# Optimization experiments

Measured on AMD Instinct MI355X. Metric: run time of the kernel, lower is better.

Reference implementation:

```python
import jax, jax.numpy as jnp
import numpy as np
import math

KV_STRIDE = 2
Q_STRIDE = 1
WAVE_LEN = 1000.0
POS_MAG = 1.0


def _pos_embed(h, w, h_kv, w_kv, q_stride, kv_stride, feat_dim):
    # Sinusoidal relative-position embeddings, matching get_position_embedding.
    h_idx = jnp.arange(h, dtype=jnp.float32) * q_stride
    w_idx = jnp.arange(w, dtype=jnp.float32) * q_stride
    h_kv_idx = jnp.arange(h_kv, dtype=jnp.float32) * kv_stride
    w_kv_idx = jnp.arange(w_kv, dtype=jnp.float32) * kv_stride
    h_diff = (h_idx[:, None] - h_kv_idx[None, :]) * POS_MAG  # (h, h_kv)
    w_diff = (w_idx[:, None] - w_kv_idx[None, :]) * POS_MAG  # (w, w_kv)
    feat_range = jnp.arange(feat_dim // 4, dtype=jnp.float32)
    dim_mat = WAVE_LEN ** (4.0 / feat_dim * feat_range)  # (feat_dim//4,)
    wd = w_diff[:, :, None] / dim_mat  # (w, w_kv, F)
    hd = h_diff[:, :, None] / dim_mat  # (h, h_kv, F)
    emb_x = jnp.concatenate([jnp.sin(wd), jnp.cos(wd)], axis=2)  # (w, w_kv, feat_dim//2)
    emb_y = jnp.concatenate([jnp.sin(hd), jnp.cos(hd)], axis=2)  # (h, h_kv, feat_dim//2)
    return emb_x, emb_y


def setup_inputs() -> dict:
    key = jax.random.key(0)
    ks = jax.random.split(key, 11)
    C = 288
    s = 1.0 / math.sqrt(C)
    return {
        'x_input': jax.random.normal(ks[0], (2, C, 64, 64), jnp.float32),
        'Wq': jax.random.normal(ks[1], (C, C), jnp.float32) * s,
        'Wk': jax.random.normal(ks[2], (C, C), jnp.float32) * s,
        'Wv': jax.random.normal(ks[3], (C, C), jnp.float32) * s,
        'Wx': jax.random.normal(ks[4], (C, C // 2), jnp.float32) * s,
        'Wy': jax.random.normal(ks[5], (C, C // 2), jnp.float32) * s,
        'Wproj': jax.random.normal(ks[6], (C, C), jnp.float32) * s,
        'bproj': jax.random.normal(ks[7], (C,), jnp.float32) * 0.02,
        'Wc': jax.random.normal(ks[8], (9, C), jnp.float32) * s,
        'bc': jax.random.normal(ks[9], (9,), jnp.float32) * 0.02,
        'gamma': jax.random.normal(ks[10], (1,), jnp.float32),
    }


def reference(x_input, Wq, Wk, Wv, Wx, Wy, Wproj, bproj, Wc, bc, gamma):
    M = Wc.shape[0]                       # num_mixtures
    n, C, h, w = x_input.shape
    d = Wq.shape[0] // M                  # qk_embed_dim (== v_dim)
    x_q = x_input                         # q_stride == 1
    x_kv = x_input[:, :, ::KV_STRIDE, ::KV_STRIDE]  # AvgPool2d(k=1, stride=2)
    h_kv, w_kv = x_kv.shape[2], x_kv.shape[3]

    # 1x1 convs as channel GEMMs
    q = jnp.einsum('nchw,oc->nohw', x_q, Wq).reshape(n, M, d, h * w)
    q = q.transpose(0, 1, 3, 2)                                    # (n,M,hw,d)
    k = jnp.einsum('nchw,oc->nohw', x_kv, Wk).reshape(n, M, d, h_kv * w_kv)

    emb_x, emb_y = _pos_embed(h, w, h_kv, w_kv, Q_STRIDE, KV_STRIDE, C)
    inv_sqrt2 = 1.0 / math.sqrt(2.0)
    pf_x = (emb_x @ Wx.T).reshape(w, w_kv, M, d).transpose(2, 0, 1, 3) * inv_sqrt2  # (M,w,w_kv,d)
    pf_y = (emb_y @ Wy.T).reshape(h, h_kv, M, d).transpose(2, 0, 1, 3) * inv_sqrt2  # (M,h,h_kv,d)

    energy = jnp.matmul(q, k).reshape(n, M, h, w, h_kv, w_kv)
    q5 = q.reshape(n, M, h, w, d)
    e_x = jnp.einsum('nmhwd,mwvd->nmhwv', q5, pf_x)  # (n,M,h,w,w_kv)
    e_y = jnp.einsum('nmhwd,mhud->nmhwu', q5, pf_y)  # (n,M,h,w,h_kv)
    energy = energy + e_x[:, :, :, :, None, :] + e_y[:, :, :, :, :, None]
    energy = energy.reshape(n, M, h * w, h_kv * w_kv)
    attn = jax.nn.softmax(energy, axis=3)

    # Learned per-mixture gating from mean query context
    context = q.transpose(0, 1, 3, 2).reshape(n, M * d, h * w).mean(axis=2)  # (n, M*d)
    mix_w = jax.nn.softmax(context @ Wc.T + bc, axis=1)                      # (n, M)
    attn = jnp.sum(attn * mix_w[:, :, None, None], axis=1)                   # (n,hw,hw_kv)

    v = jnp.einsum('nchw,oc->nohw', x_kv, Wv).reshape(n, M * d, h_kv * w_kv)
    v = v.transpose(0, 2, 1)                                                 # (n,hw_kv,M*d)
    out = jnp.matmul(attn, v).transpose(0, 2, 1).reshape(n, M * d, h, w)
    out = jnp.einsum('nchw,oc->nohw', out, Wproj) + bproj[None, :, None, None]
    return gamma[0] * out + x_input
```

## Files before the change

kernel.cpp:

```cpp
#include <hip/hip_runtime.h>
#include <math.h>

#define NB     2
#define CDIM   288
#define HW     4096
#define PKV    1024
#define MHEAD  9
#define DHEAD  32

typedef __attribute__((ext_vector_type(8))) short bf16x8;
typedef __attribute__((ext_vector_type(4))) float f32x4;

__device__ inline unsigned short f2bf(float x) {
    unsigned int u = __float_as_uint(x);
    u = (u + 0x7fffu + ((u >> 16) & 1u)) >> 16;
    return (unsigned short)u;
}


__global__ __launch_bounds__(256) void prep(const float* __restrict__ X,
        const float* __restrict__ Wq, const float* __restrict__ Wk,
        const float* __restrict__ Wv, const float* __restrict__ Wproj,
        const float* __restrict__ Wx, const float* __restrict__ Wy,
        unsigned short* __restrict__ XF, unsigned short* __restrict__ WFq,
        unsigned short* __restrict__ WFk, unsigned short* __restrict__ WFv,
        unsigned short* __restrict__ WFp, float* __restrict__ WTx,
        float* __restrict__ WTy, float* __restrict__ MX) {
    __shared__ float t32[32][33];
    __shared__ float t16[16][17];
    __shared__ float red[4];
    int b = blockIdx.x;
    int tid = threadIdx.x;
    if (b < 2304) {
        int bx = b % 128, by = (b / 128) % 9, n = b / 1152;
        int j0 = bx * 32, c0 = by * 32;
        int tx = tid & 31, ty = tid >> 5;
#pragma unroll
        for (int l = 0; l < 4; ++l) {
            int c = ty + l * 8;
            t32[c][tx] = X[((size_t)n * CDIM + c0 + c) * HW + j0 + tx];
        }
        __syncthreads();
        int s = tid >> 7;
        int u = tid & 127;
        int lane = u >> 1, e0 = (u & 1) * 4;
        int jl = s * 16 + (lane & 15);
        int cb = (lane >> 4) * 8 + e0;
        unsigned int w0 = f2bf(t32[cb + 0][jl]) | ((unsigned int)f2bf(t32[cb + 1][jl]) << 16);
        unsigned int w1 = f2bf(t32[cb + 2][jl]) | ((unsigned int)f2bf(t32[cb + 3][jl]) << 16);
        int jt = (j0 >> 4) + s, cc = c0 >> 5;
        unsigned short* O = XF + (size_t)n * HW * CDIM + ((size_t)jt * 9 + cc) * 512 + lane * 8 + e0;
        uint2 pk = { w0, w1 };
        *(uint2*)O = pk;
    } else if (b < 2628) {
        int u = b - 2304;
        int bx = u % 9, by = (u / 9) % 18, bz = u / 162;
        const float* W = bz ? Wy : Wx;
        float* WT      = bz ? WTy : WTx;
        int f0 = bx * 16, o0 = by * 16;
        int tx = tid & 15, ty = tid >> 4;
        t16[ty][tx] = W[(o0 + ty) * 144 + f0 + tx];
        __syncthreads();
        WT[(f0 + ty) * 288 + o0 + tx] = t16[tx][ty];
    } else if (b < 2790) {
        int t = b - 2628;
        int sub = tid >> 6, lane = tid & 63;
        int ot = t / 9, cc = t % 9;
        const float* W = (sub == 0) ? Wq : (sub == 1) ? Wk : (sub == 2) ? Wv : Wproj;
        unsigned short* O = ((sub == 0) ? WFq : (sub == 1) ? WFk : (sub == 2) ? WFv : WFp)
                            + (size_t)t * 512;
        int o  = ot * 16 + (lane & 15);
        int c0 = cc * 32 + (lane >> 4) * 8;
        const float* src = W + (size_t)o * CDIM + c0;
        float4 f0 = *(const float4*)src, f1 = *(const float4*)(src + 4);
        unsigned int v0 = f2bf(f0.x) | ((unsigned int)f2bf(f0.y) << 16);
        unsigned int v1 = f2bf(f0.z) | ((unsigned int)f2bf(f0.w) << 16);
        unsigned int v2 = f2bf(f1.x) | ((unsigned int)f2bf(f1.y) << 16);
        unsigned int v3 = f2bf(f1.z) | ((unsigned int)f2bf(f1.w) << 16);
        uint4 pk = { v0, v1, v2, v3 };
        *(uint4*)(O + lane * 8) = pk;
    } else {
        int bid = b - 2790;
        const float* xr = X + (size_t)bid * HW;
        float s = 0.f;
        for (int j = tid; j < HW; j += 256) s += xr[j];
        for (int off = 32; off > 0; off >>= 1) s += __shfl_xor(s, off, 64);
        if ((tid & 63) == 0) red[tid >> 6] = s;
        __syncthreads();
        if (tid == 0) MX[bid] = (red[0] + red[1] + red[2] + red[3]) * (1.f / 4096.f);
    }
}

__global__ __launch_bounds__(256) void qkv_F(const unsigned short* __restrict__ WFq,
        const unsigned short* __restrict__ WFk, const unsigned short* __restrict__ WFv,
        const unsigned short* __restrict__ XF, unsigned short* __restrict__ Qf,
        unsigned short* __restrict__ KF, unsigned short* __restrict__ VF) {
    __shared__ __attribute__((aligned(16))) unsigned short tr[4][32][40];
    int n  = blockIdx.z;
    int m  = blockIdx.y;
    int wv = threadIdx.x >> 6, lane = threadIdx.x & 63;
    int lq = lane & 15, quad = lane >> 4;
    if (blockIdx.x < 32) {
        int j0 = blockIdx.x * 128;
        int jw = j0 + wv * 32;
        const unsigned short* Wb = WFq + ((size_t)(m * 2) * 9) * 512 + lane * 8;
        const unsigned short* Xb = XF + (size_t)n * HW * CDIM + ((size_t)(jw >> 4) * 9) * 512 + lane * 8;
        f32x4 acc[2][2] = {};
#pragma unroll
        for (int cc = 0; cc < 9; ++cc) {
            bf16x8 a0 = *(const bf16x8*)(Wb + (size_t)cc * 512);
            bf16x8 a1 = *(const bf16x8*)(Wb + (size_t)(9 + cc) * 512);
            bf16x8 b0 = *(const bf16x8*)(Xb + (size_t)cc * 512);
            bf16x8 b1 = *(const bf16x8*)(Xb + (size_t)(9 + cc) * 512);
            acc[0][0] = __builtin_amdgcn_mfma_f32_16x16x32_bf16(a0, b0, acc[0][0], 0, 0, 0);
            acc[0][1] = __builtin_amdgcn_mfma_f32_16x16x32_bf16(a0, b1, acc[0][1], 0, 0, 0);
            acc[1][0] = __builtin_amdgcn_mfma_f32_16x16x32_bf16(a1, b0, acc[1][0], 0, 0, 0);
            acc[1][1] = __builtin_amdgcn_mfma_f32_16x16x32_bf16(a1, b1, acc[1][1], 0, 0, 0);
        }
#pragma unroll
        for (int oi = 0; oi < 2; ++oi)
#pragma unroll
            for (int ji = 0; ji < 2; ++ji)
#pragma unroll
                for (int r = 0; r < 4; ++r)
                    tr[wv][ji * 16 + lq][oi * 16 + quad * 4 + r] = f2bf(acc[oi][ji][r]);
        int jl = lane & 31, half = lane >> 5;
        bf16x8 v0 = *(const bf16x8*)&tr[wv][jl][half * 16];
        bf16x8 v1 = *(const bf16x8*)&tr[wv][jl][half * 16 + 8];
        unsigned short* Qm = Qf + ((size_t)(n * MHEAD + m) * HW + jw + jl) * 32 + half * 16;
        *(bf16x8*)Qm = v0;
        *(bf16x8*)(Qm + 8) = v1;
    } else {
        int p0 = (blockIdx.x - 32) * 128;
        int pw = p0 + wv * 32;
        const unsigned short* XFn = XF + (size_t)n * HW * CDIM;
        size_t bidx[2];
#pragma unroll
        for (int pi = 0; pi < 2; ++pi) {
            int p   = pw + pi * 16 + lq;
            int pos = ((p >> 5) << 7) + ((p & 31) << 1);
            bidx[pi] = ((size_t)(pos >> 4) * 9) * 512 + ((pos & 15) + 16 * quad) * 8;
        }
        const unsigned short* Wkb = WFk + ((size_t)(m * 2) * 9) * 512 + lane * 8;
        const unsigned short* Wvb = WFv + ((size_t)(m * 2) * 9) * 512 + lane * 8;
        f32x4 ak[2][2] = {}, av[2][2] = {};
#pragma unroll
        for (int cc = 0; cc < 9; ++cc) {
            bf16x8 a0k = *(const bf16x8*)(Wkb + (size_t)cc * 512);
            bf16x8 a1k = *(const bf16x8*)(Wkb + (size_t)(9 + cc) * 512);
            bf16x8 a0v = *(const bf16x8*)(Wvb + (size_t)cc * 512);
            bf16x8 a1v = *(const bf16x8*)(Wvb + (size_t)(9 + cc) * 512);
            bf16x8 b0  = *(const bf16x8*)(XFn + bidx[0] + (size_t)cc * 512);
            bf16x8 b1  = *(const bf16x8*)(XFn + bidx[1] + (size_t)cc * 512);
            ak[0][0] = __builtin_amdgcn_mfma_f32_16x16x32_bf16(a0k, b0, ak[0][0], 0, 0, 0);
            ak[0][1] = __builtin_amdgcn_mfma_f32_16x16x32_bf16(a0k, b1, ak[0][1], 0, 0, 0);
            ak[1][0] = __builtin_amdgcn_mfma_f32_16x16x32_bf16(a1k, b0, ak[1][0], 0, 0, 0);
            ak[1][1] = __builtin_amdgcn_mfma_f32_16x16x32_bf16(a1k, b1, ak[1][1], 0, 0, 0);
            av[0][0] = __builtin_amdgcn_mfma_f32_16x16x32_bf16(a0v, b0, av[0][0], 0, 0, 0);
            av[0][1] = __builtin_amdgcn_mfma_f32_16x16x32_bf16(a0v, b1, av[0][1], 0, 0, 0);
            av[1][0] = __builtin_amdgcn_mfma_f32_16x16x32_bf16(a1v, b0, av[1][0], 0, 0, 0);
            av[1][1] = __builtin_amdgcn_mfma_f32_16x16x32_bf16(a1v, b1, av[1][1], 0, 0, 0);
        }
#pragma unroll
        for (int oi = 0; oi < 2; ++oi)
#pragma unroll
            for (int pi = 0; pi < 2; ++pi)
#pragma unroll
                for (int r = 0; r < 4; ++r)
                    tr[wv][pi * 16 + lq][oi * 16 + quad * 4 + r] = f2bf(ak[oi][pi][r]);
        unsigned short* KFm = KF + (size_t)(n * MHEAD + m) * (PKV * 32);
#pragma unroll
        for (int pi = 0; pi < 2; ++pi) {
            bf16x8 v = *(const bf16x8*)&tr[wv][pi * 16 + lq][quad * 8];
            *(bf16x8*)(KFm + (size_t)((pw >> 4) + pi) * 512 + lane * 8) = v;
        }
#pragma unroll
        for (int oi = 0; oi < 2; ++oi)
#pragma unroll
            for (int pi = 0; pi < 2; ++pi)
#pragma unroll
                for (int r = 0; r < 4; ++r)
                    tr[wv][oi * 16 + quad * 4 + r][pi * 16 + lq] = f2bf(av[oi][pi][r]);
        unsigned short* VFn = VF + (size_t)n * CDIM * PKV;
#pragma unroll
        for (int oi = 0; oi < 2; ++oi) {
            bf16x8 v = *(const bf16x8*)&tr[wv][oi * 16 + lq][quad * 8];
            *(bf16x8*)(VFn + (size_t)((m * 2 + oi) * 32 + (pw >> 5)) * 512 + lane * 8) = v;
        }
    }
}

__global__ __launch_bounds__(320) void pff_kernel(const float* __restrict__ WTx,
        const float* __restrict__ WTy, float* __restrict__ FX, float* __restrict__ FY) {
    int blk  = blockIdx.x;
    int axis = blk / 126;
    int dif  = blk % 126;
    __shared__ float emb[144];
    int tid = threadIdx.x;
    float diff = (float)(dif - 62);
    if (tid < 72) {
        float dm = expf(6.9077552789821368f * ((float)tid * (1.f / 72.f)));
        float t  = diff / dm;
        emb[tid]      = sinf(t);
        emb[72 + tid] = cosf(t);
    }
    __syncthreads();
    if (tid < 288) {
        const float* WT = axis ? WTy : WTx;
        float s = 0.f;
#pragma unroll 8
        for (int f = 0; f < 144; ++f) s += emb[f] * WT[f * 288 + tid];
        int m = tid >> 5, d = tid & 31;
        float* F = axis ? FY : FX;
        F[((size_t)m * 126 + dif) * 32 + d] = s * 0.70710678118654752f;
    }
}

__global__ __launch_bounds__(256) void exey_kernel(const unsigned short* __restrict__ Qf,
        const float* __restrict__ FX, const float* __restrict__ FY,
        float* __restrict__ EX, float* __restrict__ EY) {
    int axis = blockIdx.x >> 6;
    int g    = blockIdx.x & 63;
    int m    = blockIdx.y;
    int n    = blockIdx.z;
    int tid  = threadIdx.x;
    size_t Qbase = (size_t)(n * MHEAD + m) * HW;

    __shared__ float fS[32][36];
    __shared__ unsigned int qSu[64][20];

    {
        const float* F = axis ? FY : FX;
        int v = tid >> 3, d0 = (tid & 7) * 4;
        *(float4*)&fS[v][d0] = *(const float4*)&F[((size_t)m * 126 + g + 62 - 2 * v) * 32 + d0];
    }
#pragma unroll
    for (int l = 0; l < 4; ++l) {
        int idx = tid + l * 256;
        int r = idx >> 4, c = idx & 15;
        int i = axis ? (g * 64 + r) : (r * 64 + g);
        qSu[r][c] = *(const unsigned int*)&Qf[(Qbase + i) * 32 + 2 * c];
    }
    __syncthreads();

    int r  = tid >> 2;
    int vg = tid & 3;
    float qv[32];
#pragma unroll
    for (int k = 0; k < 4; ++k) {
        uint4 qa = *(const uint4*)&qSu[r][k * 4];
        unsigned int uu[4] = { qa.x, qa.y, qa.z, qa.w };
#pragma unroll
        for (int e = 0; e < 4; ++e) {
            qv[k * 8 + 2 * e]     = __uint_as_float(uu[e] << 16);
            qv[k * 8 + 2 * e + 1] = __uint_as_float(uu[e] & 0xffff0000u);
        }
    }
    float acc8[8] = {};
#pragma unroll
    for (int k4 = 0; k4 < 8; ++k4) {
        float qx = qv[4 * k4], qy = qv[4 * k4 + 1], qz = qv[4 * k4 + 2], qw = qv[4 * k4 + 3];
#pragma unroll
        for (int t = 0; t < 8; ++t) {
            float4 f4 = *(const float4*)&fS[vg * 8 + t][k4 * 4];
            acc8[t] += qx * f4.x + qy * f4.y + qz * f4.z + qw * f4.w;
        }
    }
    int i = axis ? (g * 64 + r) : (r * 64 + g);
    float* out = axis ? EY : EX;
    size_t obase = (Qbase + i) * 32 + vg * 8;
    float4 s0 = { acc8[0], acc8[1], acc8[2], acc8[3] };
    float4 s1 = { acc8[4], acc8[5], acc8[6], acc8[7] };
    *(float4*)&out[obase]     = s0;
    *(float4*)&out[obase + 4] = s1;
}

__global__ void mixw2_kernel(const float* __restrict__ Wq, const float* __restrict__ MX,
                             const float* __restrict__ Wc, const float* __restrict__ bc,
                             float* __restrict__ MIXW) {
    __shared__ float ctx_s[NB * CDIM];
    __shared__ float lg[18];
    int tid = threadIdx.x;
    for (int p = tid; p < NB * CDIM; p += 256) {
        int n = p / CDIM, o = p % CDIM;
        const float* wr = Wq + (size_t)o * CDIM;
        const float* mx = MX + n * CDIM;
        float s = 0.f;
        for (int c = 0; c < CDIM; c += 4) {
            float4 w4 = *(const float4*)&wr[c];
            float4 m4 = *(const float4*)&mx[c];
            s += w4.x * m4.x + w4.y * m4.y + w4.z * m4.z + w4.w * m4.w;
        }
        ctx_s[p] = s;
    }
    __syncthreads();
    if (tid < 18) {
        int n = tid / 9, j = tid % 9;
        float s = bc[j];
        for (int o = 0; o < CDIM; ++o) s += ctx_s[n * CDIM + o] * Wc[j * CDIM + o];
        lg[tid] = s;
    }
    __syncthreads();
    if (tid < 2) {
        float mx = -1e30f;
        for (int j = 0; j < 9; ++j) mx = fmaxf(mx, lg[tid * 9 + j]);
        float e[9], sm = 0.f;
        for (int j = 0; j < 9; ++j) { e[j] = __expf(lg[tid * 9 + j] - mx); sm += e[j]; }
        for (int j = 0; j < 9; ++j) MIXW[tid * 9 + j] = e[j] / sm;
    }
}

__global__ __launch_bounds__(512, 4) void attn_fused(
        const unsigned short* __restrict__ Qf, const unsigned short* __restrict__ KF,
        const unsigned short* __restrict__ VF, const unsigned short* __restrict__ WFp,
        const float* __restrict__ EX, const float* __restrict__ EY,
        const float* __restrict__ MIXW, const float* __restrict__ bproj,
        const float* __restrict__ x, const float* __restrict__ gamma,
        float* __restrict__ OUT) {
    int n    = blockIdx.x >> 8;
    int i0   = (blockIdx.x & 255) * 16;
    int tid  = threadIdx.x;
    int wv   = tid >> 6;
    int lane = tid & 63;
    int lq   = lane & 15;
    int quad = lane >> 4;

    __shared__ float ext_s[16][33];
    __shared__ float eyt_s[16][33];
    __shared__ float ws_s[8][16];
    __shared__ float ltot_s[16];
    __shared__ __attribute__((aligned(16))) unsigned short tr[16][1032];
    __shared__ __attribute__((aligned(16))) unsigned short Mt[16][296];

    float mixed[8][4];
#pragma unroll
    for (int t = 0; t < 8; ++t)
#pragma unroll
        for (int j = 0; j < 4; ++j) mixed[t][j] = 0.f;

    int sq = tid >> 5, sv = tid & 31;

    for (int m = 0; m < MHEAD; ++m) {
        const unsigned short* Qm  = Qf + ((size_t)(n * MHEAD + m) * HW + i0) * 32;
        const unsigned short* KmF = KF + (size_t)(n * MHEAD + m) * (PKV * 32);
        size_t ebase = ((size_t)(n * MHEAD + m) * HW + i0 + sq) * 32 + sv;
        __syncthreads();
        ext_s[sq][sv] = EX[ebase];
        eyt_s[sq][sv] = EY[ebase];
        __syncthreads();

        bf16x8 afrag = *(const bf16x8*)(Qm + (size_t)lq * 32 + quad * 8);
        float exA[4], exB[4];
#pragma unroll
        for (int j = 0; j < 4; ++j) {
            exA[j] = ext_s[quad * 4 + j][lq];
            exB[j] = ext_s[quad * 4 + j][16 + lq];
        }

        bf16x8 bf[8];
#pragma unroll
        for (int t = 0; t < 8; ++t)
            bf[t] = *(const bf16x8*)(KmF + (size_t)(wv * 8 + t) * 512 + lane * 8);
        f32x4 acc[8];
#pragma unroll
        for (int t = 0; t < 8; ++t) acc[t] = (f32x4){0.f, 0.f, 0.f, 0.f};
#pragma unroll
        for (int t = 0; t < 8; ++t)
            acc[t] = __builtin_amdgcn_mfma_f32_16x16x32_bf16(afrag, bf[t], acc[t], 0, 0, 0);

        float rs[4] = {0.f, 0.f, 0.f, 0.f};
#pragma unroll
        for (int t = 0; t < 8; ++t) {
            int u = wv * 4 + (t >> 1);
            bool hi = t & 1;
#pragma unroll
            for (int j = 0; j < 4; ++j) {
                float e = __expf(acc[t][j] + (hi ? exB[j] : exA[j]) + eyt_s[quad * 4 + j][u]);
                rs[j] += e;
                acc[t][j] = e;
            }
        }
#pragma unroll
        for (int j = 0; j < 4; ++j) {
            rs[j] += __shfl_xor(rs[j], 1, 64);
            rs[j] += __shfl_xor(rs[j], 2, 64);
            rs[j] += __shfl_xor(rs[j], 4, 64);
            rs[j] += __shfl_xor(rs[j], 8, 64);
        }
        if (lq == 0) {
#pragma unroll
            for (int j = 0; j < 4; ++j) ws_s[wv][quad * 4 + j] = rs[j];
        }
        __syncthreads();
        if (tid < 16) {
            float s = 0.f;
#pragma unroll
            for (int w = 0; w < 8; ++w) s += ws_s[w][tid];
            ltot_s[tid] = s;
        }
        __syncthreads();

        float wm = MIXW[n * MHEAD + m];
        float fct[4];
#pragma unroll
        for (int j = 0; j < 4; ++j) fct[j] = wm / ltot_s[quad * 4 + j];
#pragma unroll
        for (int t = 0; t < 8; ++t)
#pragma unroll
            for (int j = 0; j < 4; ++j) mixed[t][j] += acc[t][j] * fct[j];
    }

#pragma unroll
    for (int t = 0; t < 8; ++t)
#pragma unroll
        for (int j = 0; j < 4; ++j)
            tr[quad * 4 + j][wv * 128 + t * 16 + lq] = f2bf(mixed[t][j]);
    __syncthreads();

    const unsigned short* VFn = VF + (size_t)n * CDIM * PKV;
    f32x4 accpv[3] = {};
#pragma unroll 4
    for (int pc = 0; pc < 32; ++pc) {
        bf16x8 pf = *(const bf16x8*)&tr[lq][pc * 32 + quad * 8];
#pragma unroll
        for (int idx = 0; idx < 3; ++idx) {
            int ot = wv + idx * 8;
            if (ot < 18) {
                bf16x8 vf = *(const bf16x8*)(VFn + (size_t)(ot * 32 + pc) * 512 + lane * 8);
                accpv[idx] = __builtin_amdgcn_mfma_f32_16x16x32_bf16(pf, vf, accpv[idx], 0, 0, 0);
            }
        }
    }
#pragma unroll
    for (int idx = 0; idx < 3; ++idx) {
        int ot = wv + idx * 8;
        if (ot < 18) {
#pragma unroll
            for (int r = 0; r < 4; ++r)
                Mt[quad * 4 + r][ot * 16 + lq] = f2bf(accpv[idx][r]);
        }
    }
    __syncthreads();

    float g = gamma[0];
#pragma unroll
    for (int idx = 0; idx < 3; ++idx) {
        int ot = wv + idx * 8;
        if (ot >= 18) continue;
        f32x4 acc = {};
#pragma unroll
        for (int cc = 0; cc < 9; ++cc) {
            bf16x8 af = *(const bf16x8*)(WFp + (size_t)(ot * 9 + cc) * 512 + lane * 8);
            bf16x8 bfm = *(const bf16x8*)&Mt[lq][cc * 32 + quad * 8];
            acc = __builtin_amdgcn_mfma_f32_16x16x32_bf16(af, bfm, acc, 0, 0, 0);
        }
#pragma unroll
        for (int r = 0; r < 4; ++r) {
            int o = ot * 16 + quad * 4 + r;
            size_t id = ((size_t)(n * CDIM) + o) * HW + i0 + lq;
            OUT[id] = g * (acc[r] + bproj[o]) + x[id];
        }
    }
}

extern "C" void kernel_launch(void* const* d_in, const int* in_sizes, int n_in,
                              void* d_out, int out_size, void* d_ws, size_t ws_size,
                              hipStream_t stream) {
    const float* x     = (const float*)d_in[0];
    const float* Wq    = (const float*)d_in[1];
    const float* Wk    = (const float*)d_in[2];
    const float* Wv    = (const float*)d_in[3];
    const float* Wx    = (const float*)d_in[4];
    const float* Wy    = (const float*)d_in[5];
    const float* Wproj = (const float*)d_in[6];
    const float* bproj = (const float*)d_in[7];
    const float* Wc    = (const float*)d_in[8];
    const float* bc    = (const float*)d_in[9];
    const float* gamma = (const float*)d_in[10];
    float* out = (float*)d_out;

    float* ws = (float*)d_ws;
    size_t off = 0;
    unsigned short* Qf  = (unsigned short*)(ws + off); off += (size_t)NB * MHEAD * HW * 32 / 2;
    unsigned short* KF  = (unsigned short*)(ws + off); off += (size_t)NB * MHEAD * PKV * 32 / 2;
    unsigned short* VF  = (unsigned short*)(ws + off); off += (size_t)NB * CDIM * PKV / 2;
    unsigned short* WFq = (unsigned short*)(ws + off); off += (size_t)CDIM * CDIM / 2;
    unsigned short* WFk = (unsigned short*)(ws + off); off += (size_t)CDIM * CDIM / 2;
    unsigned short* WFv = (unsigned short*)(ws + off); off += (size_t)CDIM * CDIM / 2;
    unsigned short* WFp = (unsigned short*)(ws + off); off += (size_t)CDIM * CDIM / 2;
    unsigned short* XF  = (unsigned short*)(ws + off); off += (size_t)NB * HW * CDIM / 2;
    float* WTx  = ws + off; off += 144 * 288;
    float* WTy  = ws + off; off += 144 * 288;
    float* FX   = ws + off; off += (size_t)MHEAD * 126 * 32;
    float* FY   = ws + off; off += (size_t)MHEAD * 126 * 32;
    float* EX   = ws + off; off += (size_t)NB * MHEAD * HW * 32;
    float* EY   = ws + off; off += (size_t)NB * MHEAD * HW * 32;
    float* MX   = ws + off; off += NB * CDIM;
    float* MIXW = ws + off; off += 32;

    prep<<<3366, 256, 0, stream>>>(x, Wq, Wk, Wv, Wproj, Wx, Wy,
                                   XF, WFq, WFk, WFv, WFp, WTx, WTy, MX);
    pff_kernel<<<252, 320, 0, stream>>>(WTx, WTy, FX, FY);
    mixw2_kernel<<<1, 256, 0, stream>>>(Wq, MX, Wc, bc, MIXW);
    qkv_F<<<dim3(40, MHEAD, NB), 256, 0, stream>>>(WFq, WFk, WFv, XF, Qf, KF, VF);
    exey_kernel<<<dim3(128, MHEAD, NB), 256, 0, stream>>>(Qf, FX, FY, EX, EY);
    attn_fused<<<NB * HW / 16, 512, 0, stream>>>(Qf, KF, VF, WFp, EX, EY, MIXW,
                                                 bproj, x, gamma, out);
}
```

Baseline: 205.1 us.

## Fuse prep-stage kernels and compute relative-position energies inside attention via MFMA

Merges the positional-feature projection, mixture-weight gating and QKV projection into one multi-role launch, cutting the launch count from six to three. The separate exey kernel and its large fp32 EX/EY buffers are removed. Instead each attention block multiplies its query fragment against bf16 position-feature tiles with MFMA and gathers the needed relative offsets from shared memory. This trades global-memory traffic and launches for extra MFMA work and shared-memory gathers inside the attention loop, and it also drops one barrier per head by summing row totals in every thread.

```diff
diff --git a/kernel.cpp b/kernel.cpp
--- a/kernel.cpp
+++ b/kernel.cpp
@@ -91,229 +91,180 @@
     }
 }
 
-__global__ __launch_bounds__(256) void qkv_F(const unsigned short* __restrict__ WFq,
-        const unsigned short* __restrict__ WFk, const unsigned short* __restrict__ WFv,
-        const unsigned short* __restrict__ XF, unsigned short* __restrict__ Qf,
-        unsigned short* __restrict__ KF, unsigned short* __restrict__ VF) {
-    __shared__ __attribute__((aligned(16))) unsigned short tr[4][32][40];
-    int n  = blockIdx.z;
-    int m  = blockIdx.y;
-    int wv = threadIdx.x >> 6, lane = threadIdx.x & 63;
-    int lq = lane & 15, quad = lane >> 4;
-    if (blockIdx.x < 32) {
-        int j0 = blockIdx.x * 128;
-        int jw = j0 + wv * 32;
-        const unsigned short* Wb = WFq + ((size_t)(m * 2) * 9) * 512 + lane * 8;
-        const unsigned short* Xb = XF + (size_t)n * HW * CDIM + ((size_t)(jw >> 4) * 9) * 512 + lane * 8;
-        f32x4 acc[2][2] = {};
-#pragma unroll
-        for (int cc = 0; cc < 9; ++cc) {
-            bf16x8 a0 = *(const bf16x8*)(Wb + (size_t)cc * 512);
-            bf16x8 a1 = *(const bf16x8*)(Wb + (size_t)(9 + cc) * 512);
-            bf16x8 b0 = *(const bf16x8*)(Xb + (size_t)cc * 512);
-            bf16x8 b1 = *(const bf16x8*)(Xb + (size_t)(9 + cc) * 512);
-            acc[0][0] = __builtin_amdgcn_mfma_f32_16x16x32_bf16(a0, b0, acc[0][0], 0, 0, 0);
-            acc[0][1] = __builtin_amdgcn_mfma_f32_16x16x32_bf16(a0, b1, acc[0][1], 0, 0, 0);
-            acc[1][0] = __builtin_amdgcn_mfma_f32_16x16x32_bf16(a1, b0, acc[1][0], 0, 0, 0);
-            acc[1][1] = __builtin_amdgcn_mfma_f32_16x16x32_bf16(a1, b1, acc[1][1], 0, 0, 0);
-        }
-#pragma unroll
-        for (int oi = 0; oi < 2; ++oi)
-#pragma unroll
-            for (int ji = 0; ji < 2; ++ji)
-#pragma unroll
-                for (int r = 0; r < 4; ++r)
-                    tr[wv][ji * 16 + lq][oi * 16 + quad * 4 + r] = f2bf(acc[oi][ji][r]);
-        int jl = lane & 31, half = lane >> 5;
-        bf16x8 v0 = *(const bf16x8*)&tr[wv][jl][half * 16];
-        bf16x8 v1 = *(const bf16x8*)&tr[wv][jl][half * 16 + 8];
-        unsigned short* Qm = Qf + ((size_t)(n * MHEAD + m) * HW + jw + jl) * 32 + half * 16;
-        *(bf16x8*)Qm = v0;
-        *(bf16x8*)(Qm + 8) = v1;
-    } else {
-        int p0 = (blockIdx.x - 32) * 128;
-        int pw = p0 + wv * 32;
-        const unsigned short* XFn = XF + (size_t)n * HW * CDIM;
-        size_t bidx[2];
-#pragma unroll
-        for (int pi = 0; pi < 2; ++pi) {
-            int p   = pw + pi * 16 + lq;
-            int pos = ((p >> 5) << 7) + ((p & 31) << 1);
-            bidx[pi] = ((size_t)(pos >> 4) * 9) * 512 + ((pos & 15) + 16 * quad) * 8;
-        }
-        const unsigned short* Wkb = WFk + ((size_t)(m * 2) * 9) * 512 + lane * 8;
-        const unsigned short* Wvb = WFv + ((size_t)(m * 2) * 9) * 512 + lane * 8;
-        f32x4 ak[2][2] = {}, av[2][2] = {};
-#pragma unroll
-        for (int cc = 0; cc < 9; ++cc) {
-            bf16x8 a0k = *(const bf16x8*)(Wkb + (size_t)cc * 512);
-            bf16x8 a1k = *(const bf16x8*)(Wkb + (size_t)(9 + cc) * 512);
-            bf16x8 a0v = *(const bf16x8*)(Wvb + (size_t)cc * 512);
-            bf16x8 a1v = *(const bf16x8*)(Wvb + (size_t)(9 + cc) * 512);
-            bf16x8 b0  = *(const bf16x8*)(XFn + bidx[0] + (size_t)cc * 512);
-            bf16x8 b1  = *(const bf16x8*)(XFn + bidx[1] + (size_t)cc * 512);
-            ak[0][0] = __builtin_amdgcn_mfma_f32_16x16x32_bf16(a0k, b0, ak[0][0], 0, 0, 0);
-            ak[0][1] = __builtin_amdgcn_mfma_f32_16x16x32_bf16(a0k, b1, ak[0][1], 0, 0, 0);
-            ak[1][0] = __builtin_amdgcn_mfma_f32_16x16x32_bf16(a1k, b0, ak[1][0], 0, 0, 0);
-            ak[1][1] = __builtin_amdgcn_mfma_f32_16x16x32_bf16(a1k, b1, ak[1][1], 0, 0, 0);
-            av[0][0] = __builtin_amdgcn_mfma_f32_16x16x32_bf16(a0v, b0, av[0][0], 0, 0, 0);
-            av[0][1] = __builtin_amdgcn_mfma_f32_16x16x32_bf16(a0v, b1, av[0][1], 0, 0, 0);
-            av[1][0] = __builtin_amdgcn_mfma_f32_16x16x32_bf16(a1v, b0, av[1][0], 0, 0, 0);
-            av[1][1] = __builtin_amdgcn_mfma_f32_16x16x32_bf16(a1v, b1, av[1][1], 0, 0, 0);
-        }
-#pragma unroll
-        for (int oi = 0; oi < 2; ++oi)
-#pragma unroll
-            for (int pi = 0; pi < 2; ++pi)
-#pragma unroll
-                for (int r = 0; r < 4; ++r)
-                    tr[wv][pi * 16 + lq][oi * 16 + quad * 4 + r] = f2bf(ak[oi][pi][r]);
-        unsigned short* KFm = KF + (size_t)(n * MHEAD + m) * (PKV * 32);
-#pragma unroll
-        for (int pi = 0; pi < 2; ++pi) {
-            bf16x8 v = *(const bf16x8*)&tr[wv][pi * 16 + lq][quad * 8];
-            *(bf16x8*)(KFm + (size_t)((pw >> 4) + pi) * 512 + lane * 8) = v;
-        }
-#pragma unroll
-        for (int oi = 0; oi < 2; ++oi)
-#pragma unroll
-            for (int pi = 0; pi < 2; ++pi)
-#pragma unroll
-                for (int r = 0; r < 4; ++r)
-                    tr[wv][oi * 16 + quad * 4 + r][pi * 16 + lq] = f2bf(av[oi][pi][r]);
-        unsigned short* VFn = VF + (size_t)n * CDIM * PKV;
-#pragma unroll
-        for (int oi = 0; oi < 2; ++oi) {
-            bf16x8 v = *(const bf16x8*)&tr[wv][oi * 16 + lq][quad * 8];
-            *(bf16x8*)(VFn + (size_t)((m * 2 + oi) * 32 + (pw >> 5)) * 512 + lane * 8) = v;
-        }
-    }
-}
-
-__global__ __launch_bounds__(320) void pff_kernel(const float* __restrict__ WTx,
-        const float* __restrict__ WTy, float* __restrict__ FX, float* __restrict__ FY) {
-    int blk  = blockIdx.x;
-    int axis = blk / 126;
-    int dif  = blk % 126;
+__global__ __launch_bounds__(256) void mid(
+        const float* __restrict__ WTx, const float* __restrict__ WTy,
+        unsigned short* __restrict__ FXb, unsigned short* __restrict__ FYb,
+        const float* __restrict__ Wq, const float* __restrict__ MX,
+        const float* __restrict__ Wc, const float* __restrict__ bc,
+        float* __restrict__ MIXW,
+        const unsigned short* __restrict__ WFq, const unsigned short* __restrict__ WFk,
+        const unsigned short* __restrict__ WFv, const unsigned short* __restrict__ XF,
+        unsigned short* __restrict__ Qf, unsigned short* __restrict__ KF,
+        unsigned short* __restrict__ VF) {
     __shared__ float emb[144];
-    int tid = threadIdx.x;
-    float diff = (float)(dif - 62);
-    if (tid < 72) {
-        float dm = expf(6.9077552789821368f * ((float)tid * (1.f / 72.f)));
-        float t  = diff / dm;
-        emb[tid]      = sinf(t);
-        emb[72 + tid] = cosf(t);
-    }
-    __syncthreads();
-    if (tid < 288) {
-        const float* WT = axis ? WTy : WTx;
-        float s = 0.f;
-#pragma unroll 8
-        for (int f = 0; f < 144; ++f) s += emb[f] * WT[f * 288 + tid];
-        int m = tid >> 5, d = tid & 31;
-        float* F = axis ? FY : FX;
-        F[((size_t)m * 126 + dif) * 32 + d] = s * 0.70710678118654752f;
-    }
-}
-
-__global__ __launch_bounds__(256) void exey_kernel(const unsigned short* __restrict__ Qf,
-        const float* __restrict__ FX, const float* __restrict__ FY,
-        float* __restrict__ EX, float* __restrict__ EY) {
-    int axis = blockIdx.x >> 6;
-    int g    = blockIdx.x & 63;
-    int m    = blockIdx.y;
-    int n    = blockIdx.z;
-    int tid  = threadIdx.x;
-    size_t Qbase = (size_t)(n * MHEAD + m) * HW;
-
-    __shared__ float fS[32][36];
-    __shared__ unsigned int qSu[64][20];
-
-    {
-        const float* F = axis ? FY : FX;
-        int v = tid >> 3, d0 = (tid & 7) * 4;
-        *(float4*)&fS[v][d0] = *(const float4*)&F[((size_t)m * 126 + g + 62 - 2 * v) * 32 + d0];
-    }
-#pragma unroll
-    for (int l = 0; l < 4; ++l) {
-        int idx = tid + l * 256;
-        int r = idx >> 4, c = idx & 15;
-        int i = axis ? (g * 64 + r) : (r * 64 + g);
-        qSu[r][c] = *(const unsigned int*)&Qf[(Qbase + i) * 32 + 2 * c];
-    }
-    __syncthreads();
-
-    int r  = tid >> 2;
-    int vg = tid & 3;
-    float qv[32];
-#pragma unroll
-    for (int k = 0; k < 4; ++k) {
-        uint4 qa = *(const uint4*)&qSu[r][k * 4];
-        unsigned int uu[4] = { qa.x, qa.y, qa.z, qa.w };
-#pragma unroll
-        for (int e = 0; e < 4; ++e) {
-            qv[k * 8 + 2 * e]     = __uint_as_float(uu[e] << 16);
-            qv[k * 8 + 2 * e + 1] = __uint_as_float(uu[e] & 0xffff0000u);
-        }
-    }
-    float acc8[8] = {};
-#pragma unroll
-    for (int k4 = 0; k4 < 8; ++k4) {
-        float qx = qv[4 * k4], qy = qv[4 * k4 + 1], qz = qv[4 * k4 + 2], qw = qv[4 * k4 + 3];
-#pragma unroll
-        for (int t = 0; t < 8; ++t) {
-            float4 f4 = *(const float4*)&fS[vg * 8 + t][k4 * 4];
-            acc8[t] += qx * f4.x + qy * f4.y + qz * f4.z + qw * f4.w;
-        }
-    }
-    int i = axis ? (g * 64 + r) : (r * 64 + g);
-    float* out = axis ? EY : EX;
-    size_t obase = (Qbase + i) * 32 + vg * 8;
-    float4 s0 = { acc8[0], acc8[1], acc8[2], acc8[3] };
-    float4 s1 = { acc8[4], acc8[5], acc8[6], acc8[7] };
-    *(float4*)&out[obase]     = s0;
-    *(float4*)&out[obase + 4] = s1;
-}
-
-__global__ void mixw2_kernel(const float* __restrict__ Wq, const float* __restrict__ MX,
-                             const float* __restrict__ Wc, const float* __restrict__ bc,
-                             float* __restrict__ MIXW) {
     __shared__ float ctx_s[NB * CDIM];
     __shared__ float lg[18];
+    __shared__ __attribute__((aligned(16))) unsigned short tr[4][32][40];
+    int b = blockIdx.x;
     int tid = threadIdx.x;
-    for (int p = tid; p < NB * CDIM; p += 256) {
-        int n = p / CDIM, o = p % CDIM;
-        const float* wr = Wq + (size_t)o * CDIM;
-        const float* mx = MX + n * CDIM;
-        float s = 0.f;
-        for (int c = 0; c < CDIM; c += 4) {
-            float4 w4 = *(const float4*)&wr[c];
-            float4 m4 = *(const float4*)&mx[c];
-            s += w4.x * m4.x + w4.y * m4.y + w4.z * m4.z + w4.w * m4.w;
-        }
-        ctx_s[p] = s;
-    }
-    __syncthreads();
-    if (tid < 18) {
-        int n = tid / 9, j = tid % 9;
-        float s = bc[j];
-        for (int o = 0; o < CDIM; ++o) s += ctx_s[n * CDIM + o] * Wc[j * CDIM + o];
-        lg[tid] = s;
-    }
-    __syncthreads();
-    if (tid < 2) {
-        float mx = -1e30f;
-        for (int j = 0; j < 9; ++j) mx = fmaxf(mx, lg[tid * 9 + j]);
-        float e[9], sm = 0.f;
-        for (int j = 0; j < 9; ++j) { e[j] = __expf(lg[tid * 9 + j] - mx); sm += e[j]; }
-        for (int j = 0; j < 9; ++j) MIXW[tid * 9 + j] = e[j] / sm;
+
+    if (b < 252) {
+        int axis = b / 126;
+        int dif  = b % 126;
+        float diff = (float)(dif - 62);
+        if (tid < 72) {
+            float dm = expf(6.9077552789821368f * ((float)tid * (1.f / 72.f)));
+            float t  = diff / dm;
+            emb[tid]      = sinf(t);
+            emb[72 + tid] = cosf(t);
+        }
+        __syncthreads();
+        const float* WT = axis ? WTy : WTx;
+        unsigned short* F = axis ? FYb : FXb;
+        for (int o = tid; o < CDIM; o += 256) {
+            float s = 0.f;
+#pragma unroll 8
+            for (int f = 0; f < 144; ++f) s += emb[f] * WT[f * 288 + o];
+            int m = o >> 5, d = o & 31;
+            F[(size_t)(m * 8 + (dif >> 4)) * 512 + ((dif & 15) + 16 * (d >> 3)) * 8 + (d & 7)]
+                = f2bf(s * 0.70710678118654752f);
+        }
+    } else if (b == 252) {
+        for (int idx = tid; idx < 1152; idx += 256) {
+            int d = idx & 31, rr = (idx >> 5) & 1, mm = (idx >> 6) % 9, ax = idx / 576;
+            int dif = 126 + rr;
+            unsigned short* F = ax ? FYb : FXb;
+            F[(size_t)(mm * 8 + 7) * 512 + ((dif & 15) + 16 * (d >> 3)) * 8 + (d & 7)] = 0;
+        }
+        for (int p = tid; p < NB * CDIM; p += 256) {
+            int n = p / CDIM, o = p % CDIM;
+            const float* wr = Wq + (size_t)o * CDIM;
+            const float* mx = MX + n * CDIM;
+            float s = 0.f;
+            for (int c = 0; c < CDIM; c += 4) {
+                float4 w4 = *(const float4*)&wr[c];
+                float4 m4 = *(const float4*)&mx[c];
+                s += w4.x * m4.x + w4.y * m4.y + w4.z * m4.z + w4.w * m4.w;
+            }
+            ctx_s[p] = s;
+        }
+        __syncthreads();
+        if (tid < 18) {
+            int n = tid / 9, j = tid % 9;
+            float s = bc[j];
+            for (int o = 0; o < CDIM; ++o) s += ctx_s[n * CDIM + o] * Wc[j * CDIM + o];
+            lg[tid] = s;
+        }
+        __syncthreads();
+        if (tid < 2) {
+            float mx = -1e30f;
+            for (int j = 0; j < 9; ++j) mx = fmaxf(mx, lg[tid * 9 + j]);
+            float e[9], sm = 0.f;
+            for (int j = 0; j < 9; ++j) { e[j] = __expf(lg[tid * 9 + j] - mx); sm += e[j]; }
+            for (int j = 0; j < 9; ++j) MIXW[tid * 9 + j] = e[j] / sm;
+        }
+    } else {
+        int bx = b - 253;
+        int gx = bx % 40;
+        int m  = (bx / 40) % 9;
+        int n  = bx / 360;
+        int wv = tid >> 6, lane = tid & 63;
+        int lq = lane & 15, quad = lane >> 4;
+        if (gx < 32) {
+            int j0 = gx * 128;
+            int jw = j0 + wv * 32;
+            const unsigned short* Wb = WFq + ((size_t)(m * 2) * 9) * 512 + lane * 8;
+            const unsigned short* Xb = XF + (size_t)n * HW * CDIM + ((size_t)(jw >> 4) * 9) * 512 + lane * 8;
+            f32x4 acc[2][2] = {};
+#pragma unroll
+            for (int cc = 0; cc < 9; ++cc) {
+                bf16x8 a0 = *(const bf16x8*)(Wb + (size_t)cc * 512);
+                bf16x8 a1 = *(const bf16x8*)(Wb + (size_t)(9 + cc) * 512);
+                bf16x8 b0 = *(const bf16x8*)(Xb + (size_t)cc * 512);
+                bf16x8 b1 = *(const bf16x8*)(Xb + (size_t)(9 + cc) * 512);
+                acc[0][0] = __builtin_amdgcn_mfma_f32_16x16x32_bf16(a0, b0, acc[0][0], 0, 0, 0);
+                acc[0][1] = __builtin_amdgcn_mfma_f32_16x16x32_bf16(a0, b1, acc[0][1], 0, 0, 0);
+                acc[1][0] = __builtin_amdgcn_mfma_f32_16x16x32_bf16(a1, b0, acc[1][0], 0, 0, 0);
+                acc[1][1] = __builtin_amdgcn_mfma_f32_16x16x32_bf16(a1, b1, acc[1][1], 0, 0, 0);
+            }
+#pragma unroll
+            for (int oi = 0; oi < 2; ++oi)
+#pragma unroll
+                for (int ji = 0; ji < 2; ++ji)
+#pragma unroll
+                    for (int r = 0; r < 4; ++r)
+                        tr[wv][ji * 16 + lq][oi * 16 + quad * 4 + r] = f2bf(acc[oi][ji][r]);
+            int jl = lane & 31, half = lane >> 5;
+            bf16x8 v0 = *(const bf16x8*)&tr[wv][jl][half * 16];
+            bf16x8 v1 = *(const bf16x8*)&tr[wv][jl][half * 16 + 8];
+            unsigned short* Qm = Qf + ((size_t)(n * MHEAD + m) * HW + jw + jl) * 32 + half * 16;
+            *(bf16x8*)Qm = v0;
+            *(bf16x8*)(Qm + 8) = v1;
+        } else {
+            int p0 = (gx - 32) * 128;
+            int pw = p0 + wv * 32;
+            const unsigned short* XFn = XF + (size_t)n * HW * CDIM;
+            size_t bidx[2];
+#pragma unroll
+            for (int pi = 0; pi < 2; ++pi) {
+                int p   = pw + pi * 16 + lq;
+                int pos = ((p >> 5) << 7) + ((p & 31) << 1);
+                bidx[pi] = ((size_t)(pos >> 4) * 9) * 512 + ((pos & 15) + 16 * quad) * 8;
+            }
+            const unsigned short* Wkb = WFk + ((size_t)(m * 2) * 9) * 512 + lane * 8;
+            const unsigned short* Wvb = WFv + ((size_t)(m * 2) * 9) * 512 + lane * 8;
+            f32x4 ak[2][2] = {}, av[2][2] = {};
+#pragma unroll
+            for (int cc = 0; cc < 9; ++cc) {
+                bf16x8 a0k = *(const bf16x8*)(Wkb + (size_t)cc * 512);
+                bf16x8 a1k = *(const bf16x8*)(Wkb + (size_t)(9 + cc) * 512);
+                bf16x8 a0v = *(const bf16x8*)(Wvb + (size_t)cc * 512);
+                bf16x8 a1v = *(const bf16x8*)(Wvb + (size_t)(9 + cc) * 512);
+                bf16x8 b0  = *(const bf16x8*)(XFn + bidx[0] + (size_t)cc * 512);
+                bf16x8 b1  = *(const bf16x8*)(XFn + bidx[1] + (size_t)cc * 512);
+                ak[0][0] = __builtin_amdgcn_mfma_f32_16x16x32_bf16(a0k, b0, ak[0][0], 0, 0, 0);
+                ak[0][1] = __builtin_amdgcn_mfma_f32_16x16x32_bf16(a0k, b1, ak[0][1], 0, 0, 0);
+                ak[1][0] = __builtin_amdgcn_mfma_f32_16x16x32_bf16(a1k, b0, ak[1][0], 0, 0, 0);
+                ak[1][1] = __builtin_amdgcn_mfma_f32_16x16x32_bf16(a1k, b1, ak[1][1], 0, 0, 0);
+                av[0][0] = __builtin_amdgcn_mfma_f32_16x16x32_bf16(a0v, b0, av[0][0], 0, 0, 0);
+                av[0][1] = __builtin_amdgcn_mfma_f32_16x16x32_bf16(a0v, b1, av[0][1], 0, 0, 0);
+                av[1][0] = __builtin_amdgcn_mfma_f32_16x16x32_bf16(a1v, b0, av[1][0], 0, 0, 0);
+                av[1][1] = __builtin_amdgcn_mfma_f32_16x16x32_bf16(a1v, b1, av[1][1], 0, 0, 0);
+            }
+#pragma unroll
+            for (int oi = 0; oi < 2; ++oi)
+#pragma unroll
+                for (int pi = 0; pi < 2; ++pi)
+#pragma unroll
+                    for (int r = 0; r < 4; ++r)
+                        tr[wv][pi * 16 + lq][oi * 16 + quad * 4 + r] = f2bf(ak[oi][pi][r]);
+            unsigned short* KFm = KF + (size_t)(n * MHEAD + m) * (PKV * 32);
+#pragma unroll
+            for (int pi = 0; pi < 2; ++pi) {
+                bf16x8 v = *(const bf16x8*)&tr[wv][pi * 16 + lq][quad * 8];
+                *(bf16x8*)(KFm + (size_t)((pw >> 4) + pi) * 512 + lane * 8) = v;
+            }
+#pragma unroll
+            for (int oi = 0; oi < 2; ++oi)
+#pragma unroll
+                for (int pi = 0; pi < 2; ++pi)
+#pragma unroll
+                    for (int r = 0; r < 4; ++r)
+                        tr[wv][oi * 16 + quad * 4 + r][pi * 16 + lq] = f2bf(av[oi][pi][r]);
+            unsigned short* VFn = VF + (size_t)n * CDIM * PKV;
+#pragma unroll
+            for (int oi = 0; oi < 2; ++oi) {
+                bf16x8 v = *(const bf16x8*)&tr[wv][oi * 16 + lq][quad * 8];
+                *(bf16x8*)(VFn + (size_t)((m * 2 + oi) * 32 + (pw >> 5)) * 512 + lane * 8) = v;
+            }
+        }
     }
 }
 
-__global__ __launch_bounds__(512, 4) void attn_fused(
+__global__ __launch_bounds__(512, 4) void attn_fused2(
         const unsigned short* __restrict__ Qf, const unsigned short* __restrict__ KF,
         const unsigned short* __restrict__ VF, const unsigned short* __restrict__ WFp,
-        const float* __restrict__ EX, const float* __restrict__ EY,
+        const unsigned short* __restrict__ FXb, const unsigned short* __restrict__ FYb,
         const float* __restrict__ MIXW, const float* __restrict__ bproj,
         const float* __restrict__ x, const float* __restrict__ gamma,
         float* __restrict__ OUT) {
@@ -325,10 +276,14 @@
     int lq   = lane & 15;
     int quad = lane >> 4;
 
-    __shared__ float ext_s[16][33];
-    __shared__ float eyt_s[16][33];
+    int bx_t = (i0 & 63) >> 4;
+    int h    = i0 >> 6;
+    int by_t = h >> 4;
+    int dh   = h & 15;
+
+    __shared__ float Rx_s[16][82];
+    __shared__ float Ry_s[16][82];
     __shared__ float ws_s[8][16];
-    __shared__ float ltot_s[16];
     __shared__ __attribute__((aligned(16))) unsigned short tr[16][1032];
     __shared__ __attribute__((aligned(16))) unsigned short Mt[16][296];
 
@@ -337,25 +292,36 @@
     for (int t = 0; t < 8; ++t)
 #pragma unroll
         for (int j = 0; j < 4; ++j) mixed[t][j] = 0.f;
-
-    int sq = tid >> 5, sv = tid & 31;
 
     for (int m = 0; m < MHEAD; ++m) {
         const unsigned short* Qm  = Qf + ((size_t)(n * MHEAD + m) * HW + i0) * 32;
         const unsigned short* KmF = KF + (size_t)(n * MHEAD + m) * (PKV * 32);
-        size_t ebase = ((size_t)(n * MHEAD + m) * HW + i0 + sq) * 32 + sv;
-        __syncthreads();
-        ext_s[sq][sv] = EX[ebase];
-        eyt_s[sq][sv] = EY[ebase];
-        __syncthreads();
-
         bf16x8 afrag = *(const bf16x8*)(Qm + (size_t)lq * 32 + quad * 8);
-        float exA[4], exB[4];
-#pragma unroll
-        for (int j = 0; j < 4; ++j) {
-            exA[j] = ext_s[quad * 4 + j][lq];
-            exB[j] = ext_s[quad * 4 + j][16 + lq];
-        }
+
+        if (wv < 5) {
+            bf16x8 bR = *(const bf16x8*)(FXb + (size_t)(m * 8 + bx_t + wv) * 512 + lane * 8);
+            f32x4 r = (f32x4){0.f, 0.f, 0.f, 0.f};
+            r = __builtin_amdgcn_mfma_f32_16x16x32_bf16(afrag, bR, r, 0, 0, 0);
+#pragma unroll
+            for (int reg = 0; reg < 4; ++reg)
+                Rx_s[quad * 4 + reg][wv * 16 + lq] = r[reg];
+        } else {
+            bf16x8 bR = *(const bf16x8*)(FYb + (size_t)(m * 8 + by_t + (wv - 5)) * 512 + lane * 8);
+            f32x4 r = (f32x4){0.f, 0.f, 0.f, 0.f};
+            r = __builtin_amdgcn_mfma_f32_16x16x32_bf16(afrag, bR, r, 0, 0, 0);
+#pragma unroll
+            for (int reg = 0; reg < 4; ++reg)
+                Ry_s[quad * 4 + reg][(wv - 5) * 16 + lq] = r[reg];
+        }
+        if (wv < 2) {
+            bf16x8 bR = *(const bf16x8*)(FYb + (size_t)(m * 8 + by_t + 3 + wv) * 512 + lane * 8);
+            f32x4 r = (f32x4){0.f, 0.f, 0.f, 0.f};
+            r = __builtin_amdgcn_mfma_f32_16x16x32_bf16(afrag, bR, r, 0, 0, 0);
+#pragma unroll
+            for (int reg = 0; reg < 4; ++reg)
+                Ry_s[quad * 4 + reg][(3 + wv) * 16 + lq] = r[reg];
+        }
+        __syncthreads();
 
         bf16x8 bf[8];
 #pragma unroll
@@ -368,16 +334,30 @@
         for (int t = 0; t < 8; ++t)
             acc[t] = __builtin_amdgcn_mfma_f32_16x16x32_bf16(afrag, bf[t], acc[t], 0, 0, 0);
 
+        float exA[4], exB[4];
+#pragma unroll
+        for (int j = 0; j < 4; ++j) {
+            int q = quad * 4 + j;
+            exA[j] = Rx_s[q][q + 62 - 2 * lq];
+            exB[j] = Rx_s[q][q + 30 - 2 * lq];
+        }
+
         float rs[4] = {0.f, 0.f, 0.f, 0.f};
 #pragma unroll
-        for (int t = 0; t < 8; ++t) {
-            int u = wv * 4 + (t >> 1);
-            bool hi = t & 1;
-#pragma unroll
-            for (int j = 0; j < 4; ++j) {
-                float e = __expf(acc[t][j] + (hi ? exB[j] : exA[j]) + eyt_s[quad * 4 + j][u]);
-                rs[j] += e;
-                acc[t][j] = e;
+        for (int tp = 0; tp < 4; ++tp) {
+            int u = wv * 4 + tp;
+            float ey[4];
+#pragma unroll
+            for (int j = 0; j < 4; ++j) ey[j] = Ry_s[quad * 4 + j][dh + 62 - 2 * u];
+#pragma unroll
+            for (int half = 0; half < 2; ++half) {
+                int t = tp * 2 + half;
+#pragma unroll
+                for (int j = 0; j < 4; ++j) {
+                    float e = __expf(acc[t][j] + (half ? exB[j] : exA[j]) + ey[j]);
+                    rs[j] += e;
+                    acc[t][j] = e;
+                }
             }
         }
 #pragma unroll
@@ -392,22 +372,18 @@
             for (int j = 0; j < 4; ++j) ws_s[wv][quad * 4 + j] = rs[j];
         }
         __syncthreads();
-        if (tid < 16) {
-            float s = 0.f;
-#pragma unroll
-            for (int w = 0; w < 8; ++w) s += ws_s[w][tid];
-            ltot_s[tid] = s;
-        }
-        __syncthreads();
 
         float wm = MIXW[n * MHEAD + m];
-        float fct[4];
-#pragma unroll
-        for (int j = 0; j < 4; ++j) fct[j] = wm / ltot_s[quad * 4 + j];
-#pragma unroll
-        for (int t = 0; t < 8; ++t)
-#pragma unroll
-            for (int j = 0; j < 4; ++j) mixed[t][j] += acc[t][j] * fct[j];
+#pragma unroll
+        for (int j = 0; j < 4; ++j) {
+            int q = quad * 4 + j;
+            float lt = 0.f;
+#pragma unroll
+            for (int w = 0; w < 8; ++w) lt += ws_s[w][q];
+            float fct = wm / lt;
+#pragma unroll
+            for (int t = 0; t < 8; ++t) mixed[t][j] += acc[t][j] * fct;
+        }
     }
 
 #pragma unroll
@@ -418,7 +394,9 @@
     __syncthreads();
 
     const unsigned short* VFn = VF + (size_t)n * CDIM * PKV;
-    f32x4 accpv[3] = {};
+    f32x4 accpv[3];
+#pragma unroll
+    for (int idx = 0; idx < 3; ++idx) accpv[idx] = (f32x4){0.f, 0.f, 0.f, 0.f};
 #pragma unroll 4
     for (int pc = 0; pc < 32; ++pc) {
         bf16x8 pf = *(const bf16x8*)&tr[lq][pc * 32 + quad * 8];
@@ -447,7 +425,7 @@
     for (int idx = 0; idx < 3; ++idx) {
         int ot = wv + idx * 8;
         if (ot >= 18) continue;
-        f32x4 acc = {};
+        f32x4 acc = (f32x4){0.f, 0.f, 0.f, 0.f};
 #pragma unroll
         for (int cc = 0; cc < 9; ++cc) {
             bf16x8 af = *(const bf16x8*)(WFp + (size_t)(ot * 9 + cc) * 512 + lane * 8);
@@ -491,19 +469,15 @@
     unsigned short* XF  = (unsigned short*)(ws + off); off += (size_t)NB * HW * CDIM / 2;
     float* WTx  = ws + off; off += 144 * 288;
     float* WTy  = ws + off; off += 144 * 288;
-    float* FX   = ws + off; off += (size_t)MHEAD * 126 * 32;
-    float* FY   = ws + off; off += (size_t)MHEAD * 126 * 32;
-    float* EX   = ws + off; off += (size_t)NB * MHEAD * HW * 32;
-    float* EY   = ws + off; off += (size_t)NB * MHEAD * HW * 32;
+    unsigned short* FXb = (unsigned short*)(ws + off); off += (size_t)MHEAD * 8 * 512 / 2;
+    unsigned short* FYb = (unsigned short*)(ws + off); off += (size_t)MHEAD * 8 * 512 / 2;
     float* MX   = ws + off; off += NB * CDIM;
     float* MIXW = ws + off; off += 32;
 
     prep<<<3366, 256, 0, stream>>>(x, Wq, Wk, Wv, Wproj, Wx, Wy,
                                    XF, WFq, WFk, WFv, WFp, WTx, WTy, MX);
-    pff_kernel<<<252, 320, 0, stream>>>(WTx, WTy, FX, FY);
-    mixw2_kernel<<<1, 256, 0, stream>>>(Wq, MX, Wc, bc, MIXW);
-    qkv_F<<<dim3(40, MHEAD, NB), 256, 0, stream>>>(WFq, WFk, WFv, XF, Qf, KF, VF);
-    exey_kernel<<<dim3(128, MHEAD, NB), 256, 0, stream>>>(Qf, FX, FY, EX, EY);
-    attn_fused<<<NB * HW / 16, 512, 0, stream>>>(Qf, KF, VF, WFp, EX, EY, MIXW,
-                                                 bproj, x, gamma, out);
+    mid<<<973, 256, 0, stream>>>(WTx, WTy, FXb, FYb, Wq, MX, Wc, bc, MIXW,
+                                 WFq, WFk, WFv, XF, Qf, KF, VF);
+    attn_fused2<<<NB * HW / 16, 512, 0, stream>>>(Qf, KF, VF, WFp, FXb, FYb, MIXW,
+                                                  bproj, x, gamma, out);
 }
```

After: 178.6 us. -13.0%, faster.
